# Performance work log

Measured on AMD Instinct MI355X. Metric: run time of the kernel, lower is better.

Reference implementation:

```python
import jax, jax.numpy as jnp
import numpy as np

N, E = 50000, 400000
HID, EDGE, NRBF = 128, 16, 32
CUTOFF = 5.0
EPS = 1e-8


def setup_inputs() -> dict:
    key = jax.random.key(0)
    ks = jax.random.split(key, 16)
    s = lambda fan_in: 1.0 / np.sqrt(fan_in)
    mlp_in = 3 * HID + NRBF + EDGE  # 432
    return {
        "h": jax.random.normal(ks[0], (N, HID), jnp.float32),
        "vec": jax.random.normal(ks[1], (N, 3, HID), jnp.float32),
        "coord": jax.random.normal(ks[2], (N, 3), jnp.float32),
        "edge_index": jax.random.randint(ks[3], (2, E), 0, N, jnp.int32),
        "edge_attr": jax.random.normal(ks[4], (E, EDGE), jnp.float32),
        "Wvp": jax.random.normal(ks[5], (HID, 3 * HID), jnp.float32) * s(HID),
        "W1": jax.random.normal(ks[6], (mlp_in, HID), jnp.float32) * s(mlp_in),
        "b1": jnp.zeros((HID,), jnp.float32),
        "W2": jax.random.normal(ks[7], (HID, HID), jnp.float32) * s(HID),
        "b2": jnp.zeros((HID,), jnp.float32),
        "W3": jax.random.normal(ks[8], (HID, 3 * HID), jnp.float32) * s(HID),
        "b3": jnp.zeros((3 * HID,), jnp.float32),
        "Wop": jax.random.normal(ks[9], (HID, 3 * HID), jnp.float32) * s(HID),
        "bop": jnp.zeros((3 * HID,), jnp.float32),
    }


def _rbf(d):
    # Gaussian smearing: centers on linspace(0, cutoff, n_rbf)
    offsets = jnp.linspace(0.0, CUTOFF, NRBF, dtype=d.dtype)
    coeff = -0.5 / (offsets[1] - offsets[0]) ** 2
    return jnp.exp(coeff * (d[:, None] - offsets) ** 2)  # [E, NRBF]


def reference(h, vec, coord, edge_index, edge_attr,
              Wvp, W1, b1, W2, b2, W3, b3, Wop, bop):
    row, col = edge_index[0], edge_index[1]
    x_ij = coord[row] - coord[col]                          # [E,3]
    d = jnp.sqrt(jnp.sum(x_ij * x_ij, axis=-1) + EPS)       # stable_norm
    d_ij = _rbf(d)                                          # [E,NRBF]

    vecp = jnp.einsum('nvh,hk->nvk', vec, Wvp)              # [N,3,3H]
    vec1, vec2, vec3 = jnp.split(vecp, 3, axis=-1)          # each [N,3,H]
    vec_dot = jnp.sum(vec1 * vec2, axis=1)                  # [N,H]

    cross = jnp.sum(vec1[row] * vec2[col], axis=1)          # [E,H]
    mlp_in = jnp.concatenate([h[row], h[col], d_ij, cross, edge_attr], axis=-1)
    x = jax.nn.silu(mlp_in @ W1 + b1)
    x = jax.nn.silu(x @ W2 + b2)
    msg = x @ W3 + b3                                       # [E,3H]
    msg_h, msg_v, msg_x = jnp.split(msg, 3, axis=1)

    h_aggr = jax.ops.segment_sum(msg_h, row, num_segments=N)           # [N,H]
    vec_msg = vec3[col] * msg_v[:, None, :] + msg_x[:, None, :] * x_ij[:, :, None]
    vec_aggr = jax.ops.segment_sum(vec_msg, row, num_segments=N)       # [N,3,H]

    o = h_aggr @ Wop + bop
    o1, o2, o3 = jnp.split(o, 3, axis=1)
    dh = vec_dot * o2 + o3
    dvec = vec3 * o1[:, None, :] + vec_aggr
    return dh, dvec
```

## Files before the change

### kernel.cpp

```cpp
#include <hip/hip_runtime.h>
#include <math.h>

constexpr int NN    = 50000;
constexpr int NE    = 400000;
constexpr int HID   = 128;

constexpr size_t OFF_VECB1 = 0;
constexpr size_t OFF_BUN  = 9600000;
constexpr size_t OFF_HAGG = 35200000;
constexpr size_t OFF_WT   = 83200000;
constexpr size_t OFF_PERM = 83421184;
constexpr size_t OFF_DEG  = 83821184;
constexpr size_t OFF_CUR  = 83871184;
constexpr size_t WS_FLOATS = 83921184;

constexpr size_t O_HWH = 0;
constexpr size_t O_HWL = 32768;
constexpr size_t O_W1H = 65536;
constexpr size_t O_W1L = 90112;
constexpr size_t O_W2H = 114688;
constexpr size_t O_W2L = 131072;
constexpr size_t O_W3H = 147456;
constexpr size_t O_W3L = 196608;
constexpr size_t O_VPH = 245760;
constexpr size_t O_VPL = 294912;
constexpr size_t O_OPH = 344064;
constexpr size_t O_OPL = 393216;

typedef __attribute__((ext_vector_type(8))) short short8;
typedef __attribute__((ext_vector_type(4))) float f32x4;

__device__ __forceinline__ short f2bf_rne(float f) {
    unsigned u = __float_as_uint(f);
    u += 0x7fffu + ((u >> 16) & 1u);
    return (short)(u >> 16);
}
__device__ __forceinline__ float bf2f(short h) {
    return __uint_as_float(((unsigned)(unsigned short)h) << 16);
}
__device__ __forceinline__ short8 tobf8(const float* t) {
    short8 r;
#pragma unroll
    for (int j = 0; j < 8; ++j) r[j] = f2bf_rne(t[j]);
    return r;
}
__device__ __forceinline__ f32x4 mfma2(short8 a, short8 bh, short8 bl, f32x4 c) {
    c = __builtin_amdgcn_mfma_f32_16x16x32_bf16(a, bh, c, 0, 0, 0);
    c = __builtin_amdgcn_mfma_f32_16x16x32_bf16(a, bl, c, 0, 0, 0);
    return c;
}

#define VLOAD8(dst, src) do { \
    *(float4*)&(dst)[0] = *(const float4*)(src); \
    *(float4*)&(dst)[4] = *(const float4*)((src) + 4); } while (0)

__global__ void misc_kernel(const float* __restrict__ W1, const float* __restrict__ W2,
                            const float* __restrict__ W3, const float* __restrict__ Wvp,
                            const float* __restrict__ Wop, short* __restrict__ wt,
                            const int* __restrict__ eidx, int* __restrict__ deg,
                            float* __restrict__ hagg, float* __restrict__ dvec)
{
    const int bid = blockIdx.x;
    const int idx = bid * 256 + threadIdx.x;
    {
        int n = idx >> 7, k = idx & 127;
        hagg[idx] = 0.f;
        size_t db = (size_t)n * 384 + k;
        dvec[db] = 0.f; dvec[db + 128] = 0.f; dvec[db + 256] = 0.f;
    }
    if (bid < 864) {
        float v; size_t oh, ol;
        if (idx < 32768) {
            int j = idx >> 7, k = idx & 127;
            v = (j < 128) ? W1[(size_t)k * 128 + j] : W1[(size_t)(128 + k) * 128 + (j - 128)];
            oh = O_HWH + idx; ol = O_HWL + idx;
        } else if (idx < 57344) {
            int l = idx - 32768; int n = l / 192, k = l - n * 192;
            int r = (k < 128) ? (288 + k) : (k < 160) ? (256 + k - 128) : (k < 176) ? (416 + k - 160) : -1;
            v = (r < 0) ? 0.f : W1[(size_t)r * 128 + n];
            oh = O_W1H + l; ol = O_W1L + l;
        } else if (idx < 73728) {
            int l = idx - 57344; int n = l >> 7, k = l & 127;
            v = W2[(size_t)k * 128 + n];
            oh = O_W2H + l; ol = O_W2L + l;
        } else if (idx < 122880) {
            int l = idx - 73728; int n = l >> 7, k = l & 127;
            v = W3[(size_t)k * 384 + n];
            oh = O_W3H + l; ol = O_W3L + l;
        } else if (idx < 172032) {
            int l = idx - 122880; int n = l >> 7, k = l & 127;
            v = Wvp[(size_t)k * 384 + n];
            oh = O_VPH + l; ol = O_VPL + l;
        } else {
            int l = idx - 172032; int n = l >> 7, k = l & 127;
            v = Wop[(size_t)k * 384 + n];
            oh = O_OPH + l; ol = O_OPL + l;
        }
        short hi = f2bf_rne(v);
        wt[oh] = hi;
        wt[ol] = f2bf_rne(v - bf2f(hi));
    }
    if (bid < 1563 && idx < NE)
        atomicAdd(&deg[eidx[idx]], 1);
}

__global__ void __launch_bounds__(1024)
sort_scan(const int* __restrict__ deg, int* __restrict__ cursor)
{
    __shared__ int part[1024];
    const int tid = threadIdx.x;
    const int base = tid * 49;
    int s = 0;
#pragma unroll 7
    for (int j = 0; j < 49; ++j) {
        int i = base + j;
        if (i < NN) s += deg[i];
    }
    part[tid] = s;
    __syncthreads();
    for (int off = 1; off < 1024; off <<= 1) {
        int v = (tid >= off) ? part[tid - off] : 0;
        __syncthreads();
        part[tid] += v;
        __syncthreads();
    }
    int run = part[tid] - s;
    for (int j = 0; j < 49; ++j) {
        int i = base + j;
        if (i < NN) { cursor[i] = run; run += deg[i]; }
    }
}

__global__ void sort_scatter(const int* __restrict__ eidx, int* __restrict__ cursor,
                             int* __restrict__ perm)
{
    int e = blockIdx.x * 256 + threadIdx.x;
    if (e < NE) {
        int pos = atomicAdd(&cursor[eidx[e]], 1);
        perm[pos] = e;
    }
}

__global__ void __launch_bounds__(256, 3)
gemm_vp(const float* __restrict__ A, int M,
        const short* __restrict__ wh, const short* __restrict__ wl,
        short* __restrict__ vecb1, short* __restrict__ bun)
{
    const int tid = threadIdx.x, wave = tid >> 6, lane = tid & 63;
    const int m = lane & 15, kg = lane >> 4;
    const int gm0 = blockIdx.x * 32;
    const int nb = wave * 96;
    const f32x4 zf = {0.f, 0.f, 0.f, 0.f};
    f32x4 acc[2][6];
#pragma unroll
    for (int mt = 0; mt < 2; ++mt)
#pragma unroll
        for (int tt = 0; tt < 6; ++tt) acc[mt][tt] = zf;

    for (int ks = 0; ks < 4; ++ks) {
        short8 ah[2];
#pragma unroll
        for (int mt = 0; mt < 2; ++mt) {
            int r = gm0 + mt * 16 + m;
            if (r >= M) r = M - 1;
            float tmp[8];
            VLOAD8(tmp, A + (size_t)r * 128 + ks * 32 + kg * 8);
            ah[mt] = tobf8(tmp);
        }
#pragma unroll
        for (int tt = 0; tt < 6; ++tt) {
            size_t wo = (size_t)(nb + tt * 16 + m) * 128 + ks * 32 + kg * 8;
            short8 bh = *(const short8*)(wh + wo);
            short8 bl = *(const short8*)(wl + wo);
#pragma unroll
            for (int mt = 0; mt < 2; ++mt)
                acc[mt][tt] = mfma2(ah[mt], bh, bl, acc[mt][tt]);
        }
    }
#pragma unroll
    for (int mt = 0; mt < 2; ++mt)
#pragma unroll
        for (int r = 0; r < 4; ++r) {
            int row = gm0 + mt * 16 + kg * 4 + r;
            if (row >= M) continue;
            int n = row / 3, v = row - n * 3;
            size_t f1 = (size_t)n * 384 + (size_t)v * 128;
            size_t b2 = (size_t)n * 1024 + (size_t)v * 128;
            size_t b3 = (size_t)n * 1024 + 384 + (size_t)v * 128;
#pragma unroll
            for (int tt = 0; tt < 6; ++tt) {
                int col = nb + tt * 16 + m;
                float val = acc[mt][tt][r];
                int seg = col >> 7, k = col & 127;
                if (seg == 0)      vecb1[f1 + k] = f2bf_rne(val);
                else if (seg == 1) bun[b2 + k] = f2bf_rne(val);
                else               bun[b3 + k] = f2bf_rne(val);
            }
        }
}

__global__ void __launch_bounds__(256, 3)
gemm_hw(const float* __restrict__ A, int M,
        const short* __restrict__ wh, const short* __restrict__ wl,
        short* __restrict__ bun)
{
    const int tid = threadIdx.x, wave = tid >> 6, lane = tid & 63;
    const int m = lane & 15, kg = lane >> 4;
    const int gm0 = blockIdx.x * 32;
    const int nb = wave * 64;
    const f32x4 zf = {0.f, 0.f, 0.f, 0.f};
    f32x4 acc[2][4];
#pragma unroll
    for (int mt = 0; mt < 2; ++mt)
#pragma unroll
        for (int tt = 0; tt < 4; ++tt) acc[mt][tt] = zf;

    for (int ks = 0; ks < 4; ++ks) {
        short8 ah[2];
#pragma unroll
        for (int mt = 0; mt < 2; ++mt) {
            int r = gm0 + mt * 16 + m;
            if (r >= M) r = M - 1;
            float tmp[8];
            VLOAD8(tmp, A + (size_t)r * 128 + ks * 32 + kg * 8);
            ah[mt] = tobf8(tmp);
        }
#pragma unroll
        for (int tt = 0; tt < 4; ++tt) {
            size_t wo = (size_t)(nb + tt * 16 + m) * 128 + ks * 32 + kg * 8;
            short8 bh = *(const short8*)(wh + wo);
            short8 bl = *(const short8*)(wl + wo);
#pragma unroll
            for (int mt = 0; mt < 2; ++mt)
                acc[mt][tt] = mfma2(ah[mt], bh, bl, acc[mt][tt]);
        }
    }
#pragma unroll
    for (int mt = 0; mt < 2; ++mt)
#pragma unroll
        for (int r = 0; r < 4; ++r) {
            int row = gm0 + mt * 16 + kg * 4 + r;
            if (row >= M) continue;
#pragma unroll
            for (int tt = 0; tt < 4; ++tt) {
                int col = nb + tt * 16 + m;
                bun[(size_t)row * 1024 + 768 + col] = f2bf_rne(acc[mt][tt][r]);
            }
        }
}

__global__ void __launch_bounds__(256, 3)
gemm_fin(const float* __restrict__ hagg, const short* __restrict__ vecb1,
         const short* __restrict__ bun,
         const short* __restrict__ wh, const short* __restrict__ wl,
         const float* __restrict__ bop, float* __restrict__ dh,
         float* __restrict__ dvec, int M)
{
    const int tid = threadIdx.x, wave = tid >> 6, lane = tid & 63;
    const int m = lane & 15, kg = lane >> 4;
    const int gm0 = blockIdx.x * 32;
    const int nb = wave * 32;
    const f32x4 zf = {0.f, 0.f, 0.f, 0.f};
    f32x4 acc[2][6];
#pragma unroll
    for (int mt = 0; mt < 2; ++mt)
#pragma unroll
        for (int t = 0; t < 6; ++t) acc[mt][t] = zf;

    for (int ks = 0; ks < 4; ++ks) {
        short8 ah[2];
#pragma unroll
        for (int mt = 0; mt < 2; ++mt) {
            int r = gm0 + mt * 16 + m;
            if (r >= M) r = M - 1;
            float tmp[8];
            VLOAD8(tmp, hagg + (size_t)r * 128 + ks * 32 + kg * 8);
            ah[mt] = tobf8(tmp);
        }
#pragma unroll
        for (int seg = 0; seg < 3; ++seg)
#pragma unroll
            for (int tt = 0; tt < 2; ++tt) {
                size_t wo = (size_t)(seg * 128 + nb + tt * 16 + m) * 128 + ks * 32 + kg * 8;
                short8 bh = *(const short8*)(wh + wo);
                short8 bl = *(const short8*)(wl + wo);
#pragma unroll
                for (int mt = 0; mt < 2; ++mt)
                    acc[mt][seg * 2 + tt] = mfma2(ah[mt], bh, bl, acc[mt][seg * 2 + tt]);
            }
    }
    float bo[3][2];
#pragma unroll
    for (int seg = 0; seg < 3; ++seg)
#pragma unroll
        for (int tt = 0; tt < 2; ++tt) bo[seg][tt] = bop[seg * 128 + nb + tt * 16 + m];

#pragma unroll
    for (int mt = 0; mt < 2; ++mt)
#pragma unroll
        for (int r = 0; r < 4; ++r) {
            int row = gm0 + mt * 16 + kg * 4 + r;
            if (row >= M) continue;
            size_t f1 = (size_t)row * 384;
            size_t b2 = (size_t)row * 1024;
            size_t bb = (size_t)row * 1024 + 384;
#pragma unroll
            for (int tt = 0; tt < 2; ++tt) {
                int k = nb + tt * 16 + m;
                float o1 = acc[mt][0 * 2 + tt][r] + bo[0][tt];
                float o2 = acc[mt][1 * 2 + tt][r] + bo[1][tt];
                float o3 = acc[mt][2 * 2 + tt][r] + bo[2][tt];
                float vd = bf2f(vecb1[f1 + k])       * bf2f(bun[b2 + k])
                         + bf2f(vecb1[f1 + 128 + k]) * bf2f(bun[b2 + 128 + k])
                         + bf2f(vecb1[f1 + 256 + k]) * bf2f(bun[b2 + 256 + k]);
                dh[(size_t)row * 128 + k] = vd * o2 + o3;
                size_t db = (size_t)row * 384 + k;
                dvec[db]       += bf2f(bun[bb + k])       * o1;
                dvec[db + 128] += bf2f(bun[bb + 128 + k]) * o1;
                dvec[db + 256] += bf2f(bun[bb + 256 + k]) * o1;
            }
        }
}

__global__ void __launch_bounds__(256, 4)
edge_kernel(const short* __restrict__ vecb1, const short* __restrict__ bun,
            const float* __restrict__ coord, const int* __restrict__ eidx,
            const float* __restrict__ eattr, const short* __restrict__ wt,
            const int* __restrict__ perm,
            const float* __restrict__ b1, const float* __restrict__ b2,
            const float* __restrict__ b3,
            float* __restrict__ hagg, float* __restrict__ dvec)
{
    __shared__ __align__(16) unsigned char smem[36864];
    short (*xh)[136]  = (short(*)[136])(&smem[0]);
    __shared__ int   s_row[64], s_col[64], s_es[64];
    __shared__ float s_xij[64][3];
    __shared__ float s_d[64];

    const int nwg = gridDim.x;
    const int q8 = nwg >> 3, r8 = nwg & 7;
    const int xcd = blockIdx.x & 7, loc = blockIdx.x >> 3;
    const int lb = (xcd < r8 ? xcd * (q8 + 1) : r8 * (q8 + 1) + (xcd - r8) * q8) + loc;

    const int tid = threadIdx.x;
    const int wave = tid >> 6, lane = tid & 63;
    const int m = lane & 15, kg = lane >> 4;
    const int nb = wave * 32;
    const int eb = lb * 64;
    const int be = tid >> 2;
    const int bq = (tid & 3) * 8;

    if (tid < 64) {
        int es = perm[eb + tid];
        int r = eidx[es], c = eidx[NE + es];
        s_es[tid] = es; s_row[tid] = r; s_col[tid] = c;
        float x0 = coord[r * 3 + 0] - coord[c * 3 + 0];
        float x1 = coord[r * 3 + 1] - coord[c * 3 + 1];
        float x2 = coord[r * 3 + 2] - coord[c * 3 + 2];
        s_xij[tid][0] = x0; s_xij[tid][1] = x1; s_xij[tid][2] = x2;
        s_d[tid] = sqrtf(x0 * x0 + x1 * x1 + x2 * x2 + 1e-8f);
    }
    __syncthreads();

    const f32x4 zf = {0.f, 0.f, 0.f, 0.f};
    const float delta = 5.0f / 31.0f;
    const float coeff = -0.5f / (delta * delta);
    const int brow = s_row[be], bcol = s_col[be], bes = s_es[be];

    float pE[8];
    short8 rB0, rB1, rB2, cB0, cB1, cB2;
    auto issue = [&](int ks) {
        if (ks < 4) {
            int kk = ks * 32 + bq;
            const short* vr = vecb1 + (size_t)brow * 384 + kk;
            const short* vc = bun + (size_t)bcol * 1024 + kk;
            rB0 = *(const short8*)(vr);
            rB1 = *(const short8*)(vr + 128);
            rB2 = *(const short8*)(vr + 256);
            cB0 = *(const short8*)(vc);
            cB1 = *(const short8*)(vc + 128);
            cB2 = *(const short8*)(vc + 256);
        } else if (ks == 5) {
            if (bq < 16) VLOAD8(pE, eattr + (size_t)bes * 16 + bq);
        }
    };
    auto commit = [&](int ks, int buf) {
        short (*cab)[40] = (short(*)[40])(&smem[(size_t)buf * 5120]);
        float tmp[8];
        if (ks < 4) {
#pragma unroll
            for (int j = 0; j < 8; ++j)
                tmp[j] = bf2f(rB0[j]) * bf2f(cB0[j])
                       + bf2f(rB1[j]) * bf2f(cB1[j])
                       + bf2f(rB2[j]) * bf2f(cB2[j]);
        } else if (ks == 4) {
            float dd = s_d[be];
#pragma unroll
            for (int j = 0; j < 8; ++j) {
                float x = dd - (float)(bq + j) * delta;
                tmp[j] = __expf(coeff * x * x);
            }
        } else {
#pragma unroll
            for (int j = 0; j < 8; ++j) tmp[j] = (bq < 16) ? pE[j] : 0.f;
        }
        *(short8*)&cab[be][bq] = tobf8(tmp);
    };

    f32x4 acc[4][2];
#pragma unroll
    for (int mt = 0; mt < 4; ++mt) { acc[mt][0] = zf; acc[mt][1] = zf; }

    issue(0); commit(0, 0);
    __syncthreads();
    for (int ks = 0; ks < 6; ++ks) {
        if (ks < 5) issue(ks + 1);
        const short (*rab)[40] = (const short(*)[40])(&smem[(size_t)(ks & 1) * 5120]);
        short8 ah4[4];
#pragma unroll
        for (int mt = 0; mt < 4; ++mt)
            ah4[mt] = *(const short8*)&rab[mt * 16 + m][kg * 8];
#pragma unroll
        for (int tt = 0; tt < 2; ++tt) {
            size_t wo = (size_t)(nb + tt * 16 + m) * 192 + ks * 32 + kg * 8;
            short8 bh = *(const short8*)(wt + O_W1H + wo);
            short8 bl = *(const short8*)(wt + O_W1L + wo);
#pragma unroll
            for (int mt = 0; mt < 4; ++mt)
                acc[mt][tt] = mfma2(ah4[mt], bh, bl, acc[mt][tt]);
        }
        if (ks < 5) commit(ks + 1, (ks + 1) & 1);
        __syncthreads();
    }

    {
        float b1v[2] = { b1[nb + m], b1[nb + 16 + m] };
#pragma unroll
        for (int mt = 0; mt < 4; ++mt) {
            float hb[4][4];
#pragma unroll
            for (int r = 0; r < 4; ++r) {
                int e = mt * 16 + kg * 4 + r;
                const short* hr = bun + (size_t)s_row[e] * 1024 + 768;
                const short* hc = bun + (size_t)s_col[e] * 1024 + 896;
                hb[r][0] = bf2f(hr[nb + m]);      hb[r][1] = bf2f(hc[nb + m]);
                hb[r][2] = bf2f(hr[nb + 16 + m]); hb[r][3] = bf2f(hc[nb + 16 + m]);
            }
#pragma unroll
            for (int r = 0; r < 4; ++r) {
                int e = mt * 16 + kg * 4 + r;
#pragma unroll
                for (int tt = 0; tt < 2; ++tt) {
                    int n = nb + tt * 16 + m;
                    float v = acc[mt][tt][r] + hb[r][tt * 2] + hb[r][tt * 2 + 1] + b1v[tt];
                    float sv = v * __builtin_amdgcn_rcpf(1.f + __expf(-v));
                    xh[e][n] = f2bf_rne(sv);
                }
            }
        }
    }
    __syncthreads();

#pragma unroll
    for (int mt = 0; mt < 4; ++mt) { acc[mt][0] = zf; acc[mt][1] = zf; }
    for (int ks = 0; ks < 4; ++ks) {
        short8 ah4[4];
#pragma unroll
        for (int mt = 0; mt < 4; ++mt)
            ah4[mt] = *(const short8*)&xh[mt * 16 + m][ks * 32 + kg * 8];
#pragma unroll
        for (int tt = 0; tt < 2; ++tt) {
            size_t wo = (size_t)(nb + tt * 16 + m) * 128 + ks * 32 + kg * 8;
            short8 bh = *(const short8*)(wt + O_W2H + wo);
            short8 bl = *(const short8*)(wt + O_W2L + wo);
#pragma unroll
            for (int mt = 0; mt < 4; ++mt)
                acc[mt][tt] = mfma2(ah4[mt], bh, bl, acc[mt][tt]);
        }
    }
    {
        float b2v[2] = { b2[nb + m], b2[nb + 16 + m] };
#pragma unroll
        for (int mt = 0; mt < 4; ++mt)
#pragma unroll
            for (int tt = 0; tt < 2; ++tt)
#pragma unroll
                for (int r = 0; r < 4; ++r) {
                    float v = acc[mt][tt][r] + b2v[tt];
                    acc[mt][tt][r] = v * __builtin_amdgcn_rcpf(1.f + __expf(-v));
                }
    }
    __syncthreads();
#pragma unroll
    for (int mt = 0; mt < 4; ++mt)
#pragma unroll
        for (int tt = 0; tt < 2; ++tt)
#pragma unroll
            for (int r = 0; r < 4; ++r) {
                int e = mt * 16 + kg * 4 + r;
                int n = nb + tt * 16 + m;
                xh[e][n] = f2bf_rne(acc[mt][tt][r]);
            }
    __syncthreads();

    float msgv[4][2][4];
    for (int c = 0; c < 3; ++c) {
        f32x4 a3[4][2];
#pragma unroll
        for (int mt = 0; mt < 4; ++mt) { a3[mt][0] = zf; a3[mt][1] = zf; }
        for (int ks = 0; ks < 4; ++ks) {
            short8 ah4[4];
#pragma unroll
            for (int mt = 0; mt < 4; ++mt)
                ah4[mt] = *(const short8*)&xh[mt * 16 + m][ks * 32 + kg * 8];
#pragma unroll
            for (int tt = 0; tt < 2; ++tt) {
                size_t wo = (size_t)(c * 128 + nb + tt * 16 + m) * 128 + ks * 32 + kg * 8;
                short8 bh = *(const short8*)(wt + O_W3H + wo);
                short8 bl = *(const short8*)(wt + O_W3L + wo);
#pragma unroll
                for (int mt = 0; mt < 4; ++mt)
                    a3[mt][tt] = mfma2(ah4[mt], bh, bl, a3[mt][tt]);
            }
        }
        float bv[2] = { b3[c * 128 + nb + m], b3[c * 128 + nb + 16 + m] };
        const int n0 = nb + m, n1 = nb + 16 + m;
        if (c == 0) {
            int cur = s_row[kg * 4];
            float s0 = 0.f, s1 = 0.f;
#pragma unroll
            for (int mt = 0; mt < 4; ++mt)
#pragma unroll
                for (int r = 0; r < 4; ++r) {
                    int rr = s_row[mt * 16 + kg * 4 + r];
                    float v0 = a3[mt][0][r] + bv[0];
                    float v1 = a3[mt][1][r] + bv[1];
                    if (rr != cur) {
                        atomicAdd(&hagg[(size_t)cur * 128 + n0], s0);
                        atomicAdd(&hagg[(size_t)cur * 128 + n1], s1);
                        cur = rr; s0 = 0.f; s1 = 0.f;
                    }
                    s0 += v0; s1 += v1;
                }
            atomicAdd(&hagg[(size_t)cur * 128 + n0], s0);
            atomicAdd(&hagg[(size_t)cur * 128 + n1], s1);
        } else if (c == 1) {
#pragma unroll
            for (int mt = 0; mt < 4; ++mt)
#pragma unroll
                for (int tt = 0; tt < 2; ++tt)
#pragma unroll
                    for (int r = 0; r < 4; ++r)
                        msgv[mt][tt][r] = a3[mt][tt][r] + bv[tt];
        } else {
            int cur = s_row[kg * 4];
            float sd[6] = {0.f, 0.f, 0.f, 0.f, 0.f, 0.f};
#pragma unroll
            for (int mt = 0; mt < 4; ++mt) {
                float v3b[4][6];
#pragma unroll
                for (int r = 0; r < 4; ++r) {
                    int e = mt * 16 + kg * 4 + r;
                    const short* v3 = bun + (size_t)s_col[e] * 1024 + 384;
                    v3b[r][0] = bf2f(v3[n0]); v3b[r][1] = bf2f(v3[128 + n0]); v3b[r][2] = bf2f(v3[256 + n0]);
                    v3b[r][3] = bf2f(v3[n1]); v3b[r][4] = bf2f(v3[128 + n1]); v3b[r][5] = bf2f(v3[256 + n1]);
                }
#pragma unroll
                for (int r = 0; r < 4; ++r) {
                    int e = mt * 16 + kg * 4 + r;
                    int rr = s_row[e];
                    if (rr != cur) {
                        float* dst = dvec + (size_t)cur * 384;
                        atomicAdd(dst + n0,       sd[0]);
                        atomicAdd(dst + 128 + n0, sd[1]);
                        atomicAdd(dst + 256 + n0, sd[2]);
                        atomicAdd(dst + n1,       sd[3]);
                        atomicAdd(dst + 128 + n1, sd[4]);
                        atomicAdd(dst + 256 + n1, sd[5]);
                        cur = rr;
#pragma unroll
                        for (int q = 0; q < 6; ++q) sd[q] = 0.f;
                    }
                    const float xj0 = s_xij[e][0], xj1 = s_xij[e][1], xj2 = s_xij[e][2];
                    float mx0 = a3[mt][0][r] + bv[0], mx1 = a3[mt][1][r] + bv[1];
                    float mv0 = msgv[mt][0][r],       mv1 = msgv[mt][1][r];
                    sd[0] += v3b[r][0] * mv0 + xj0 * mx0;
                    sd[1] += v3b[r][1] * mv0 + xj1 * mx0;
                    sd[2] += v3b[r][2] * mv0 + xj2 * mx0;
                    sd[3] += v3b[r][3] * mv1 + xj0 * mx1;
                    sd[4] += v3b[r][4] * mv1 + xj1 * mx1;
                    sd[5] += v3b[r][5] * mv1 + xj2 * mx1;
                }
            }
            float* dst = dvec + (size_t)cur * 384;
            atomicAdd(dst + n0,       sd[0]);
            atomicAdd(dst + 128 + n0, sd[1]);
            atomicAdd(dst + 256 + n0, sd[2]);
            atomicAdd(dst + n1,       sd[3]);
            atomicAdd(dst + 128 + n1, sd[4]);
            atomicAdd(dst + 256 + n1, sd[5]);
        }
    }
}

extern "C" void kernel_launch(void* const* d_in, const int* in_sizes, int n_in,
                              void* d_out, int out_size, void* d_ws, size_t ws_size,
                              hipStream_t stream)
{
    const float* h     = (const float*)d_in[0];
    const float* vec   = (const float*)d_in[1];
    const float* coord = (const float*)d_in[2];
    const int*   eidx  = (const int*)  d_in[3];
    const float* eattr = (const float*)d_in[4];
    const float* Wvp   = (const float*)d_in[5];
    const float* W1    = (const float*)d_in[6];
    const float* b1    = (const float*)d_in[7];
    const float* W2    = (const float*)d_in[8];
    const float* b2    = (const float*)d_in[9];
    const float* W3    = (const float*)d_in[10];
    const float* b3    = (const float*)d_in[11];
    const float* Wop   = (const float*)d_in[12];
    const float* bop   = (const float*)d_in[13];

    if (ws_size < WS_FLOATS * sizeof(float)) return;

    float* ws    = (float*)d_ws;
    short* vecb1 = (short*)(ws + OFF_VECB1);
    short* bun   = (short*)(ws + OFF_BUN);
    float* hagg  = ws + OFF_HAGG;
    short* wt    = (short*)(ws + OFF_WT);
    int*   perm  = (int*)(ws + OFF_PERM);
    int*   deg   = (int*)(ws + OFF_DEG);
    int*   cur   = (int*)(ws + OFF_CUR);
    float* dh    = (float*)d_out;
    float* dvec  = (float*)d_out + (size_t)NN * HID;

    dim3 b256(256);
    hipMemsetAsync(deg, 0, NN * sizeof(int), stream);
    misc_kernel<<<25000, b256, 0, stream>>>(W1, W2, W3, Wvp, Wop, wt, eidx, deg, hagg, dvec);
    sort_scan<<<1, 1024, 0, stream>>>(deg, cur);
    sort_scatter<<<1563, b256, 0, stream>>>(eidx, cur, perm);
    gemm_vp<<<4688, b256, 0, stream>>>(vec, 150000, wt + O_VPH, wt + O_VPL, vecb1, bun);
    gemm_hw<<<1563, b256, 0, stream>>>(h, 50000, wt + O_HWH, wt + O_HWL, bun);
    edge_kernel<<<6250, b256, 0, stream>>>(vecb1, bun, coord, eidx, eattr, wt, perm,
                                           b1, b2, b3, hagg, dvec);
    gemm_fin<<<1563, b256, 0, stream>>>(hagg, vecb1, bun, wt + O_OPH, wt + O_OPL,
                                        bop, dh, dvec, 50000);
}
```

Baseline: 1.196 ms.

## Stage full layer-1 input tile in LDS and prefetch gathers across edge kernel

The layer-1 A operand (cross products, RBF, edge attributes) is now built in one 198-wide LDS tile before the MFMA loop, using double-buffered gathers, instead of a per-k-step double-buffered pipeline with a barrier each step. The h_row/h_col bias gathers and the vec3 gathers are software-prefetched one or two m-tiles ahead. The W3 output stage is split so that msg_v and msg_x are computed per m-tile together, with no msgv array held across chunks. The aim is fewer barriers and more hidden gather latency, at the cost of higher register pressure, which could hurt occupancy under the 4-wave launch bound.

```diff
diff --git a/kernel.cpp b/kernel.cpp
--- a/kernel.cpp
+++ b/kernel.cpp
@@ -332,7 +332,8 @@
             float* __restrict__ hagg, float* __restrict__ dvec)
 {
     __shared__ __align__(16) unsigned char smem[36864];
-    short (*xh)[136]  = (short(*)[136])(&smem[0]);
+    short (*Amat)[198] = (short(*)[198])(&smem[0]);
+    short (*xh)[136]   = (short(*)[136])(&smem[0]);
     __shared__ int   s_row[64], s_col[64], s_es[64];
     __shared__ float s_xij[64][3];
     __shared__ float s_d[64];
@@ -368,58 +369,72 @@
     const int brow = s_row[be], bcol = s_col[be], bes = s_es[be];
 
     float pE[8];
-    short8 rB0, rB1, rB2, cB0, cB1, cB2;
-    auto issue = [&](int ks) {
-        if (ks < 4) {
-            int kk = ks * 32 + bq;
-            const short* vr = vecb1 + (size_t)brow * 384 + kk;
-            const short* vc = bun + (size_t)bcol * 1024 + kk;
-            rB0 = *(const short8*)(vr);
-            rB1 = *(const short8*)(vr + 128);
-            rB2 = *(const short8*)(vr + 256);
-            cB0 = *(const short8*)(vc);
-            cB1 = *(const short8*)(vc + 128);
-            cB2 = *(const short8*)(vc + 256);
-        } else if (ks == 5) {
-            if (bq < 16) VLOAD8(pE, eattr + (size_t)bes * 16 + bq);
-        }
+    if (bq < 16) VLOAD8(pE, eattr + (size_t)bes * 16 + bq);
+    short8 rA[3], cA[3], rB[3], cB[3];
+    auto issueV = [&](int ks, short8* rr, short8* cc) {
+        int kk = ks * 32 + bq;
+        const short* vr = vecb1 + (size_t)brow * 384 + kk;
+        const short* vc = bun + (size_t)bcol * 1024 + kk;
+        rr[0] = *(const short8*)(vr);
+        rr[1] = *(const short8*)(vr + 128);
+        rr[2] = *(const short8*)(vr + 256);
+        cc[0] = *(const short8*)(vc);
+        cc[1] = *(const short8*)(vc + 128);
+        cc[2] = *(const short8*)(vc + 256);
     };
-    auto commit = [&](int ks, int buf) {
-        short (*cab)[40] = (short(*)[40])(&smem[(size_t)buf * 5120]);
+    auto commitV = [&](int ks, const short8* rr, const short8* cc) {
         float tmp[8];
-        if (ks < 4) {
-#pragma unroll
-            for (int j = 0; j < 8; ++j)
-                tmp[j] = bf2f(rB0[j]) * bf2f(cB0[j])
-                       + bf2f(rB1[j]) * bf2f(cB1[j])
-                       + bf2f(rB2[j]) * bf2f(cB2[j]);
-        } else if (ks == 4) {
-            float dd = s_d[be];
-#pragma unroll
-            for (int j = 0; j < 8; ++j) {
-                float x = dd - (float)(bq + j) * delta;
-                tmp[j] = __expf(coeff * x * x);
-            }
-        } else {
-#pragma unroll
-            for (int j = 0; j < 8; ++j) tmp[j] = (bq < 16) ? pE[j] : 0.f;
-        }
-        *(short8*)&cab[be][bq] = tobf8(tmp);
+#pragma unroll
+        for (int j = 0; j < 8; ++j)
+            tmp[j] = bf2f(rr[0][j]) * bf2f(cc[0][j])
+                   + bf2f(rr[1][j]) * bf2f(cc[1][j])
+                   + bf2f(rr[2][j]) * bf2f(cc[2][j]);
+        *(short8*)&Amat[be][ks * 32 + bq] = tobf8(tmp);
     };
+    issueV(0, rA, cA); issueV(1, rB, cB);
+    commitV(0, rA, cA); issueV(2, rA, cA);
+    commitV(1, rB, cB); issueV(3, rB, cB);
+    commitV(2, rA, cA);
+    commitV(3, rB, cB);
+    {
+        float dd = s_d[be], tmp[8];
+#pragma unroll
+        for (int j = 0; j < 8; ++j) {
+            float x = dd - (float)(bq + j) * delta;
+            tmp[j] = __expf(coeff * x * x);
+        }
+        *(short8*)&Amat[be][128 + bq] = tobf8(tmp);
+    }
+    {
+        float tmp[8];
+#pragma unroll
+        for (int j = 0; j < 8; ++j) tmp[j] = (bq < 16) ? pE[j] : 0.f;
+        *(short8*)&Amat[be][160 + bq] = tobf8(tmp);
+    }
+    __syncthreads();
+
+    float hbA[4][4], hbB[4][4];
+    auto loadHB = [&](int mt, float (*hb)[4]) {
+#pragma unroll
+        for (int r = 0; r < 4; ++r) {
+            int e = mt * 16 + kg * 4 + r;
+            const short* hr = bun + (size_t)s_row[e] * 1024 + 768;
+            const short* hc = bun + (size_t)s_col[e] * 1024 + 896;
+            hb[r][0] = bf2f(hr[nb + m]);      hb[r][1] = bf2f(hc[nb + m]);
+            hb[r][2] = bf2f(hr[nb + 16 + m]); hb[r][3] = bf2f(hc[nb + 16 + m]);
+        }
+    };
+    loadHB(0, hbA);
 
     f32x4 acc[4][2];
 #pragma unroll
     for (int mt = 0; mt < 4; ++mt) { acc[mt][0] = zf; acc[mt][1] = zf; }
-
-    issue(0); commit(0, 0);
-    __syncthreads();
+#pragma unroll
     for (int ks = 0; ks < 6; ++ks) {
-        if (ks < 5) issue(ks + 1);
-        const short (*rab)[40] = (const short(*)[40])(&smem[(size_t)(ks & 1) * 5120]);
         short8 ah4[4];
 #pragma unroll
         for (int mt = 0; mt < 4; ++mt)
-            ah4[mt] = *(const short8*)&rab[mt * 16 + m][kg * 8];
+            ah4[mt] = *(const short8*)&Amat[mt * 16 + m][ks * 32 + kg * 8];
 #pragma unroll
         for (int tt = 0; tt < 2; ++tt) {
             size_t wo = (size_t)(nb + tt * 16 + m) * 192 + ks * 32 + kg * 8;
@@ -429,30 +444,22 @@
             for (int mt = 0; mt < 4; ++mt)
                 acc[mt][tt] = mfma2(ah4[mt], bh, bl, acc[mt][tt]);
         }
-        if (ks < 5) commit(ks + 1, (ks + 1) & 1);
-        __syncthreads();
-    }
+    }
+    __syncthreads();
 
     {
         float b1v[2] = { b1[nb + m], b1[nb + 16 + m] };
 #pragma unroll
         for (int mt = 0; mt < 4; ++mt) {
-            float hb[4][4];
+            float (*hbC)[4] = (mt & 1) ? hbB : hbA;
+            if (mt < 3) loadHB(mt + 1, (mt & 1) ? hbA : hbB);
 #pragma unroll
             for (int r = 0; r < 4; ++r) {
                 int e = mt * 16 + kg * 4 + r;
-                const short* hr = bun + (size_t)s_row[e] * 1024 + 768;
-                const short* hc = bun + (size_t)s_col[e] * 1024 + 896;
-                hb[r][0] = bf2f(hr[nb + m]);      hb[r][1] = bf2f(hc[nb + m]);
-                hb[r][2] = bf2f(hr[nb + 16 + m]); hb[r][3] = bf2f(hc[nb + 16 + m]);
-            }
-#pragma unroll
-            for (int r = 0; r < 4; ++r) {
-                int e = mt * 16 + kg * 4 + r;
 #pragma unroll
                 for (int tt = 0; tt < 2; ++tt) {
                     int n = nb + tt * 16 + m;
-                    float v = acc[mt][tt][r] + hb[r][tt * 2] + hb[r][tt * 2 + 1] + b1v[tt];
+                    float v = acc[mt][tt][r] + hbC[r][tt * 2] + hbC[r][tt * 2 + 1] + b1v[tt];
                     float sv = v * __builtin_amdgcn_rcpf(1.f + __expf(-v));
                     xh[e][n] = f2bf_rne(sv);
                 }
@@ -503,8 +510,20 @@
             }
     __syncthreads();
 
-    float msgv[4][2][4];
-    for (int c = 0; c < 3; ++c) {
+    const int n0 = nb + m, n1 = nb + 16 + m;
+    float v3bA[4][6], v3bB[4][6];
+    auto loadV3 = [&](int mt, float (*vb)[6]) {
+#pragma unroll
+        for (int r = 0; r < 4; ++r) {
+            int e = mt * 16 + kg * 4 + r;
+            const short* v3 = bun + (size_t)s_col[e] * 1024 + 384;
+            vb[r][0] = bf2f(v3[n0]); vb[r][1] = bf2f(v3[128 + n0]); vb[r][2] = bf2f(v3[256 + n0]);
+            vb[r][3] = bf2f(v3[n1]); vb[r][4] = bf2f(v3[128 + n1]); vb[r][5] = bf2f(v3[256 + n1]);
+        }
+    };
+    loadV3(0, v3bA); loadV3(1, v3bB);
+
+    {
         f32x4 a3[4][2];
 #pragma unroll
         for (int mt = 0; mt < 4; ++mt) { a3[mt][0] = zf; a3[mt][1] = zf; }
@@ -515,7 +534,7 @@
                 ah4[mt] = *(const short8*)&xh[mt * 16 + m][ks * 32 + kg * 8];
 #pragma unroll
             for (int tt = 0; tt < 2; ++tt) {
-                size_t wo = (size_t)(c * 128 + nb + tt * 16 + m) * 128 + ks * 32 + kg * 8;
+                size_t wo = (size_t)(nb + tt * 16 + m) * 128 + ks * 32 + kg * 8;
                 short8 bh = *(const short8*)(wt + O_W3H + wo);
                 short8 bl = *(const short8*)(wt + O_W3L + wo);
 #pragma unroll
@@ -523,83 +542,85 @@
                     a3[mt][tt] = mfma2(ah4[mt], bh, bl, a3[mt][tt]);
             }
         }
-        float bv[2] = { b3[c * 128 + nb + m], b3[c * 128 + nb + 16 + m] };
-        const int n0 = nb + m, n1 = nb + 16 + m;
-        if (c == 0) {
-            int cur = s_row[kg * 4];
-            float s0 = 0.f, s1 = 0.f;
-#pragma unroll
-            for (int mt = 0; mt < 4; ++mt)
-#pragma unroll
-                for (int r = 0; r < 4; ++r) {
-                    int rr = s_row[mt * 16 + kg * 4 + r];
-                    float v0 = a3[mt][0][r] + bv[0];
-                    float v1 = a3[mt][1][r] + bv[1];
-                    if (rr != cur) {
-                        atomicAdd(&hagg[(size_t)cur * 128 + n0], s0);
-                        atomicAdd(&hagg[(size_t)cur * 128 + n1], s1);
-                        cur = rr; s0 = 0.f; s1 = 0.f;
-                    }
-                    s0 += v0; s1 += v1;
+        float bv[2] = { b3[nb + m], b3[nb + 16 + m] };
+        int cur = s_row[kg * 4];
+        float s0 = 0.f, s1 = 0.f;
+#pragma unroll
+        for (int mt = 0; mt < 4; ++mt)
+#pragma unroll
+            for (int r = 0; r < 4; ++r) {
+                int rr = s_row[mt * 16 + kg * 4 + r];
+                float v0 = a3[mt][0][r] + bv[0];
+                float v1 = a3[mt][1][r] + bv[1];
+                if (rr != cur) {
+                    atomicAdd(&hagg[(size_t)cur * 128 + n0], s0);
+                    atomicAdd(&hagg[(size_t)cur * 128 + n1], s1);
+                    cur = rr; s0 = 0.f; s1 = 0.f;
                 }
-            atomicAdd(&hagg[(size_t)cur * 128 + n0], s0);
-            atomicAdd(&hagg[(size_t)cur * 128 + n1], s1);
-        } else if (c == 1) {
-#pragma unroll
-            for (int mt = 0; mt < 4; ++mt)
-#pragma unroll
-                for (int tt = 0; tt < 2; ++tt)
-#pragma unroll
-                    for (int r = 0; r < 4; ++r)
-                        msgv[mt][tt][r] = a3[mt][tt][r] + bv[tt];
-        } else {
-            int cur = s_row[kg * 4];
-            float sd[6] = {0.f, 0.f, 0.f, 0.f, 0.f, 0.f};
-#pragma unroll
-            for (int mt = 0; mt < 4; ++mt) {
-                float v3b[4][6];
-#pragma unroll
-                for (int r = 0; r < 4; ++r) {
-                    int e = mt * 16 + kg * 4 + r;
-                    const short* v3 = bun + (size_t)s_col[e] * 1024 + 384;
-                    v3b[r][0] = bf2f(v3[n0]); v3b[r][1] = bf2f(v3[128 + n0]); v3b[r][2] = bf2f(v3[256 + n0]);
-                    v3b[r][3] = bf2f(v3[n1]); v3b[r][4] = bf2f(v3[128 + n1]); v3b[r][5] = bf2f(v3[256 + n1]);
+                s0 += v0; s1 += v1;
+            }
+        atomicAdd(&hagg[(size_t)cur * 128 + n0], s0);
+        atomicAdd(&hagg[(size_t)cur * 128 + n1], s1);
+    }
+
+    {
+        float bv1[2] = { b3[128 + nb + m], b3[128 + nb + 16 + m] };
+        float bv2[2] = { b3[256 + nb + m], b3[256 + nb + 16 + m] };
+        int cur = s_row[kg * 4];
+        float sd[6] = {0.f, 0.f, 0.f, 0.f, 0.f, 0.f};
+#pragma unroll
+        for (int mt = 0; mt < 4; ++mt) {
+            f32x4 a1[2], a2[2];
+            a1[0] = zf; a1[1] = zf; a2[0] = zf; a2[1] = zf;
+#pragma unroll
+            for (int ks = 0; ks < 4; ++ks) {
+                short8 ah = *(const short8*)&xh[mt * 16 + m][ks * 32 + kg * 8];
+#pragma unroll
+                for (int tt = 0; tt < 2; ++tt) {
+                    size_t wo1 = (size_t)(128 + nb + tt * 16 + m) * 128 + ks * 32 + kg * 8;
+                    size_t wo2 = (size_t)(256 + nb + tt * 16 + m) * 128 + ks * 32 + kg * 8;
+                    a1[tt] = mfma2(ah, *(const short8*)(wt + O_W3H + wo1),
+                                       *(const short8*)(wt + O_W3L + wo1), a1[tt]);
+                    a2[tt] = mfma2(ah, *(const short8*)(wt + O_W3H + wo2),
+                                       *(const short8*)(wt + O_W3L + wo2), a2[tt]);
                 }
-#pragma unroll
-                for (int r = 0; r < 4; ++r) {
-                    int e = mt * 16 + kg * 4 + r;
-                    int rr = s_row[e];
-                    if (rr != cur) {
-                        float* dst = dvec + (size_t)cur * 384;
-                        atomicAdd(dst + n0,       sd[0]);
-                        atomicAdd(dst + 128 + n0, sd[1]);
-                        atomicAdd(dst + 256 + n0, sd[2]);
-                        atomicAdd(dst + n1,       sd[3]);
-                        atomicAdd(dst + 128 + n1, sd[4]);
-                        atomicAdd(dst + 256 + n1, sd[5]);
-                        cur = rr;
-#pragma unroll
-                        for (int q = 0; q < 6; ++q) sd[q] = 0.f;
-                    }
-                    const float xj0 = s_xij[e][0], xj1 = s_xij[e][1], xj2 = s_xij[e][2];
-                    float mx0 = a3[mt][0][r] + bv[0], mx1 = a3[mt][1][r] + bv[1];
-                    float mv0 = msgv[mt][0][r],       mv1 = msgv[mt][1][r];
-                    sd[0] += v3b[r][0] * mv0 + xj0 * mx0;
-                    sd[1] += v3b[r][1] * mv0 + xj1 * mx0;
-                    sd[2] += v3b[r][2] * mv0 + xj2 * mx0;
-                    sd[3] += v3b[r][3] * mv1 + xj0 * mx1;
-                    sd[4] += v3b[r][4] * mv1 + xj1 * mx1;
-                    sd[5] += v3b[r][5] * mv1 + xj2 * mx1;
+            }
+            float (*vb)[6] = (mt & 1) ? v3bB : v3bA;
+#pragma unroll
+            for (int r = 0; r < 4; ++r) {
+                int e = mt * 16 + kg * 4 + r;
+                int rr = s_row[e];
+                if (rr != cur) {
+                    float* dst = dvec + (size_t)cur * 384;
+                    atomicAdd(dst + n0,       sd[0]);
+                    atomicAdd(dst + 128 + n0, sd[1]);
+                    atomicAdd(dst + 256 + n0, sd[2]);
+                    atomicAdd(dst + n1,       sd[3]);
+                    atomicAdd(dst + 128 + n1, sd[4]);
+                    atomicAdd(dst + 256 + n1, sd[5]);
+                    cur = rr;
+#pragma unroll
+                    for (int q = 0; q < 6; ++q) sd[q] = 0.f;
                 }
-            }
-            float* dst = dvec + (size_t)cur * 384;
-            atomicAdd(dst + n0,       sd[0]);
-            atomicAdd(dst + 128 + n0, sd[1]);
-            atomicAdd(dst + 256 + n0, sd[2]);
-            atomicAdd(dst + n1,       sd[3]);
-            atomicAdd(dst + 128 + n1, sd[4]);
-            atomicAdd(dst + 256 + n1, sd[5]);
-        }
+                const float xj0 = s_xij[e][0], xj1 = s_xij[e][1], xj2 = s_xij[e][2];
+                float mv0 = a1[0][r] + bv1[0], mv1 = a1[1][r] + bv1[1];
+                float mx0 = a2[0][r] + bv2[0], mx1 = a2[1][r] + bv2[1];
+                sd[0] += vb[r][0] * mv0 + xj0 * mx0;
+                sd[1] += vb[r][1] * mv0 + xj1 * mx0;
+                sd[2] += vb[r][2] * mv0 + xj2 * mx0;
+                sd[3] += vb[r][3] * mv1 + xj0 * mx1;
+                sd[4] += vb[r][4] * mv1 + xj1 * mx1;
+                sd[5] += vb[r][5] * mv1 + xj2 * mx1;
+            }
+            if (mt < 2) loadV3(mt + 2, vb);
+        }
+        float* dst = dvec + (size_t)cur * 384;
+        atomicAdd(dst + n0,       sd[0]);
+        atomicAdd(dst + 128 + n0, sd[1]);
+        atomicAdd(dst + 256 + n0, sd[2]);
+        atomicAdd(dst + n1,       sd[3]);
+        atomicAdd(dst + 128 + n1, sd[4]);
+        atomicAdd(dst + 256 + n1, sd[5]);
     }
 }
 
```

Result: slower. 1.569 ms (+31.2%).
